# Optimization experiments

Hardware: AMD Instinct MI355X
Metric: run time of the kernel (lower is better)

Reference implementation:

```python
import jax, jax.numpy as jnp
import numpy as np
from jax import lax

B, HS, WS, C, NH, WIN = 32, 56, 56, 192, 6, 7
HID = int(C * 4.0)
EPS = 1e-5


def _ln(x, g, b):
    m = jnp.mean(x, -1, keepdims=True)
    v = jnp.mean((x - m) ** 2, -1, keepdims=True)
    return (x - m) * jax.lax.rsqrt(v + EPS) * g + b


def _cpe(x, H, W, w, b):
    # x: [B, H*W, C]; depthwise 3x3 conv positional encoding, residual add
    Bn = x.shape[0]
    feat = x.reshape(Bn, H, W, C).transpose(0, 3, 1, 2)  # NCHW
    out = lax.conv_general_dilated(feat, w, (1, 1), 'SAME',
                                   feature_group_count=C,
                                   dimension_numbers=('NCHW', 'OIHW', 'NCHW'))
    out = out + b[None, :, None, None]
    pos = out.transpose(0, 2, 3, 1).reshape(Bn, H * W, C)
    return x + pos


def _window_attn(xw, qkv_w, qkv_b, proj_w, proj_b):
    # xw: [nW, N, C]; faithful einops split 'b n (d k h) -> k b h n d'
    nW, N, _ = xw.shape
    hd = C // NH
    qkv = xw @ qkv_w + qkv_b                      # [nW, N, 3C]
    qkv = qkv.reshape(nW, N, hd, 3, NH)           # (d k h) split
    q, k, v = jnp.moveaxis(qkv.transpose(3, 0, 4, 1, 2), 0, 0)  # each [nW, NH, N, hd]
    scale = hd ** -0.5
    scores = jnp.einsum('bhid,bhjd->bhij', q, k) * scale
    attn = jax.nn.softmax(scores, axis=-1)
    out = jnp.einsum('bhij,bhjd->bhid', attn, v)  # [nW, NH, N, hd]
    out = out.transpose(0, 2, 1, 3).reshape(nW, N, C)  # 'b h n d -> b n (h d)'
    return out @ proj_w + proj_b


def _forward(x, H, W, cpe0_w, cpe0_b, cpe1_w, cpe1_b, n1_g, n1_b,
             qkv_w, qkv_b, proj_w, proj_b, n2_g, n2_b,
             fc1_w, fc1_b, fc2_w, fc2_b):
    Bn = x.shape[0]
    shortcut = _cpe(x, H, W, cpe0_w, cpe0_b)
    y = _ln(shortcut, n1_g, n1_b).reshape(Bn, H, W, C)
    pad_r = (WIN - W % WIN) % WIN
    pad_b = (WIN - H % WIN) % WIN
    y = jnp.pad(y, ((0, 0), (0, pad_b), (0, pad_r), (0, 0)))
    Hp, Wp = H + pad_b, W + pad_r
    nh, nw = Hp // WIN, Wp // WIN
    # faithful: 'b (w_h nw_h) (w_w nw_w) c -> (b nw_h nw_w) (w_h w_w) c'
    y = y.reshape(Bn, WIN, nh, WIN, nw, C).transpose(0, 2, 4, 1, 3, 5)
    y = y.reshape(Bn * nh * nw, WIN * WIN, C)
    y = _window_attn(y, qkv_w, qkv_b, proj_w, proj_b)
    # reverse: '(b nw_h nw_w) (w_h w_w) c -> b (w_h nw_h) (w_w nw_w) c'
    y = y.reshape(Bn, nh, nw, WIN, WIN, C).transpose(0, 3, 1, 4, 2, 5)
    y = y.reshape(Bn, Hp, Wp, C)[:, :H, :W, :].reshape(Bn, H * W, C)
    y = shortcut + y
    y = _cpe(y, H, W, cpe1_w, cpe1_b)
    h = _ln(y, n2_g, n2_b)
    h = jax.nn.gelu(h @ fc1_w + fc1_b, approximate=False) @ fc2_w + fc2_b
    return y + h


def setup_inputs() -> dict:
    key = jax.random.key(0)
    ks = jax.random.split(key, 12)
    s = 0.02
    return {
        'x': jax.random.normal(ks[0], (B, HS * WS, C), jnp.float32),
        'H': HS, 'W': WS,
        'cpe0_w': jax.random.normal(ks[1], (C, 1, 3, 3), jnp.float32) * s,
        'cpe0_b': jnp.zeros((C,), jnp.float32),
        'cpe1_w': jax.random.normal(ks[2], (C, 1, 3, 3), jnp.float32) * s,
        'cpe1_b': jnp.zeros((C,), jnp.float32),
        'n1_g': jnp.ones((C,), jnp.float32), 'n1_b': jnp.zeros((C,), jnp.float32),
        'qkv_w': jax.random.normal(ks[3], (C, 3 * C), jnp.float32) * s,
        'qkv_b': jnp.zeros((3 * C,), jnp.float32),
        'proj_w': jax.random.normal(ks[4], (C, C), jnp.float32) * s,
        'proj_b': jnp.zeros((C,), jnp.float32),
        'n2_g': jnp.ones((C,), jnp.float32), 'n2_b': jnp.zeros((C,), jnp.float32),
        'fc1_w': jax.random.normal(ks[5], (C, HID), jnp.float32) * s,
        'fc1_b': jnp.zeros((HID,), jnp.float32),
        'fc2_w': jax.random.normal(ks[6], (HID, C), jnp.float32) * s,
        'fc2_b': jnp.zeros((C,), jnp.float32),
    }


def reference(x, H, W, cpe0_w, cpe0_b, cpe1_w, cpe1_b, n1_g, n1_b,
              qkv_w, qkv_b, proj_w, proj_b, n2_g, n2_b,
              fc1_w, fc1_b, fc2_w, fc2_b):
    return _forward(x, H, W, cpe0_w, cpe0_b, cpe1_w, cpe1_b, n1_g, n1_b,
                    qkv_w, qkv_b, proj_w, proj_b, n2_g, n2_b,
                    fc1_w, fc1_b, fc2_w, fc2_b)
```

## Files before the change

### kernel.cpp

```cpp
#include <hip/hip_runtime.h>
#include <hip/hip_bf16.h>
#include <math.h>

#define Bn   32
#define Hh   56
#define Wd   56
#define Cc   192
#define NHh  6
#define HDim 32
#define HIDN 768
#define Tt   (Bn*Hh*Wd)
#define NWIN (Bn*64)

typedef __attribute__((ext_vector_type(8))) short short8;
typedef __attribute__((ext_vector_type(4))) short s4v;
typedef __attribute__((ext_vector_type(4))) float floatx4;

__device__ __forceinline__ short f2bf(float f) {
    unsigned u = __float_as_uint(f);
    u += 0x7fffu + ((u >> 16) & 1u);
    return (short)(u >> 16);
}
__device__ __forceinline__ float bf2f(short s) {
    return __uint_as_float(((unsigned)(unsigned short)s) << 16);
}

__device__ __forceinline__ void gl_lds16(const short* g, short* l) {
    __builtin_amdgcn_global_load_lds(
        (const __attribute__((address_space(1))) unsigned int*)g,
        (__attribute__((address_space(3))) unsigned int*)l,
        16, 0, 0);
}

__device__ __forceinline__ int xcd_swz(int bid, int nb) {
    return (bid & 7) * (nb >> 3) + (bid >> 3);
}

__global__ void k_transpose(const float* __restrict__ W, short* __restrict__ WT,
                            int K, int N) {
    int idx = blockIdx.x * 256 + threadIdx.x;
    if (idx >= K * N) return;
    int n = idx / K, k = idx % K;
    WT[idx] = f2bf(W[k * N + n]);
}

__global__ void k_transpose_qkv(const float* __restrict__ W, short* __restrict__ WT) {
    int idx = blockIdx.x * 256 + threadIdx.x;
    if (idx >= 192 * 576) return;
    int n = idx / 192, kk = idx % 192;
    int d = n & 31, hh = (n >> 5) % 6, k3 = n / 192;
    int oc = d * 18 + k3 * 6 + hh;
    WT[idx] = f2bf(W[kk * 576 + oc]);
}

template<int ADDP>
__global__ void __launch_bounds__(256) k_cpe_ln(
    const float* __restrict__ xin, const float* __restrict__ wconv,
    const float* __restrict__ bconv, const float* __restrict__ g,
    const float* __restrict__ beta, float* __restrict__ ysum_out,
    short* __restrict__ ln_out, int windowed, const short* __restrict__ proj)
{
    const int lane = threadIdx.x & 63;
    const int wv   = threadIdx.x >> 6;
    const bool act = lane < 48;
    const int c4   = (lane < 48 ? lane : lane - 16) * 4;

    const floatx4 zf = {0.f, 0.f, 0.f, 0.f};
    float wreg[36];
    #pragma unroll
    for (int i = 0; i < 9; ++i)
        *(floatx4*)&wreg[i * 4] = *(const floatx4*)(wconv + c4 * 9 + i * 4);
    const floatx4 gv  = *(const floatx4*)(g + c4);
    const floatx4 bv  = *(const floatx4*)(beta + c4);
    const floatx4 bcv = *(const floatx4*)(bconv + c4);

    const int W = xcd_swz(blockIdx.x, gridDim.x) * 4 + wv;
    const int b = W / (Hh * 7);
    const int rem = W % (Hh * 7);
    const int h = rem / 7, wslot = rem % 7;
    const int w0 = wslot * 8;

    floatx4 r[3][10];
    const int hy0 = (h > 0) ? h - 1 : 0;
    const int hy2 = (h < Hh - 1) ? h + 1 : Hh - 1;
    const int hys[3] = {hy0, h, hy2};
    #pragma unroll
    for (int dy = 0; dy < 3; ++dy) {
        const int hy = hys[dy];
        const float* rp = xin + ((size_t)b * (Hh * Wd) + hy * Wd) * Cc + c4;
        #pragma unroll
        for (int j = 0; j < 10; ++j) {
            int wx = w0 - 1 + j;
            int wc = (wx < 0) ? 0 : ((wx > Wd - 1) ? Wd - 1 : wx);
            floatx4 v = *(const floatx4*)(rp + wc * Cc);
            if (ADDP) {
                int prow = (b * 64 + (hy & 7) * 8 + (wc & 7)) * 49
                         + (hy >> 3) * 7 + (wc >> 3);
                s4v pv = *(const s4v*)(proj + (size_t)prow * Cc + c4);
                #pragma unroll
                for (int q = 0; q < 4; ++q) v[q] += bf2f(pv[q]);
            }
            r[dy][j] = v;
        }
    }
    if (h == 0) {
        #pragma unroll
        for (int j = 0; j < 10; ++j) r[0][j] = zf;
    }
    if (h == Hh - 1) {
        #pragma unroll
        for (int j = 0; j < 10; ++j) r[2][j] = zf;
    }
    if (w0 == 0)      { r[0][0] = zf; r[1][0] = zf; r[2][0] = zf; }
    if (w0 == Wd - 8) { r[0][9] = zf; r[1][9] = zf; r[2][9] = zf; }

    floatx4 val[8];
    #pragma unroll
    for (int tk = 0; tk < 8; ++tk) {
        floatx4 a = bcv;
        #pragma unroll
        for (int dy = 0; dy < 3; ++dy) {
            #pragma unroll
            for (int dx = 0; dx < 3; ++dx) {
                const int t = dy * 3 + dx;
                floatx4 v = r[dy][tk + dx];
                #pragma unroll
                for (int j = 0; j < 4; ++j)
                    a[j] += wreg[j * 9 + t] * v[j];
            }
        }
        floatx4 xc = r[1][tk + 1];
        #pragma unroll
        for (int j = 0; j < 4; ++j) val[tk][j] = xc[j] + a[j];
    }

    float s[8], s2[8];
    #pragma unroll
    for (int tk = 0; tk < 8; ++tk) {
        float a = val[tk][0] + val[tk][1] + val[tk][2] + val[tk][3];
        float a2 = val[tk][0]*val[tk][0] + val[tk][1]*val[tk][1]
                 + val[tk][2]*val[tk][2] + val[tk][3]*val[tk][3];
        s[tk]  = act ? a  : 0.f;
        s2[tk] = act ? a2 : 0.f;
    }
    #pragma unroll
    for (int off = 1; off < 64; off <<= 1) {
        #pragma unroll
        for (int tk = 0; tk < 8; ++tk) {
            s[tk]  += __shfl_xor(s[tk],  off, 64);
            s2[tk] += __shfl_xor(s2[tk], off, 64);
        }
    }

    const int blk0 = (b * Hh + h) * Wd + w0;
    #pragma unroll
    for (int tk = 0; tk < 8; ++tk) {
        const float mean = s[tk] * (1.0f / Cc);
        const float var  = s2[tk] * (1.0f / Cc) - mean * mean;
        const float rs   = rsqrtf(var + 1e-5f);
        int rr;
        if (windowed) {
            int win = b * 64 + (h & 7) * 8 + tk;
            int pos = (h >> 3) * 7 + wslot;
            rr = win * 49 + pos;
        } else {
            rr = blk0 + tk;
        }
        if (act) {
            *(floatx4*)(ysum_out + (size_t)(blk0 + tk) * Cc + c4) = val[tk];
            s4v o;
            #pragma unroll
            for (int j = 0; j < 4; ++j)
                o[j] = f2bf((val[tk][j] - mean) * rs * gv[j] + bv[j]);
            *(s4v*)(ln_out + (size_t)rr * Cc + c4) = o;
        }
    }
}

template<int K, int EPI>
__global__ void __launch_bounds__(256) k_gemm_tiled(
    const short* __restrict__ A, const short* __restrict__ BT,
    const float* __restrict__ bias, void* __restrict__ outp)
{
    __shared__ __align__(16) short As[128 * 32];
    __shared__ __align__(16) short Bs[64 * 32];
    const int tid = threadIdx.x;
    const int gx = gridDim.x;
    const int flat = blockIdx.y * gx + blockIdx.x;
    const int swz = xcd_swz(flat, gx * gridDim.y);
    const int n0 = (swz % gx) * 64;
    const int m0 = (swz / gx) * 128;
    const int w = tid >> 6, lane = tid & 63;
    const int lcol = lane & 15, quad = lane >> 4;

    floatx4 acc[2][4];
    #pragma unroll
    for (int mi = 0; mi < 2; ++mi)
        #pragma unroll
        for (int ni = 0; ni < 4; ++ni) acc[mi][ni] = (floatx4){0, 0, 0, 0};

    const int ar = tid >> 2;
    const int ac = (((tid & 3) ^ ((tid >> 2) & 3) ^ ((tid >> 4) & 3)) * 8);
    const short* agp  = A + (size_t)(m0 + ar) * K + ac;
    const short* agp2 = A + (size_t)(m0 + 64 + ar) * K + ac;
    const short* bgp  = BT + (size_t)(n0 + ar) * K + ac;
    short* asw = As + tid * 8;
    short* bsw = Bs + tid * 8;

    const int rsz = (quad ^ (lcol & 3) ^ ((lcol >> 2) & 3)) * 8;
    const short* ard0 = As + (w * 32 + lcol) * 32 + rsz;
    const short* ard1 = As + (w * 32 + 16 + lcol) * 32 + rsz;
    const short* brd  = Bs + lcol * 32 + rsz;

    for (int k0 = 0; k0 < K; k0 += 32) {
        __syncthreads();
        gl_lds16(agp + k0, asw);
        gl_lds16(agp2 + k0, asw + 64 * 32);
        gl_lds16(bgp + k0, bsw);
        __syncthreads();
        short8 a0 = *(const short8*)ard0;
        short8 a1 = *(const short8*)ard1;
        #pragma unroll
        for (int ni = 0; ni < 4; ++ni) {
            short8 b = *(const short8*)(brd + ni * 16 * 32);
            acc[0][ni] = __builtin_amdgcn_mfma_f32_16x16x32_bf16(a0, b, acc[0][ni], 0, 0, 0);
            acc[1][ni] = __builtin_amdgcn_mfma_f32_16x16x32_bf16(a1, b, acc[1][ni], 0, 0, 0);
        }
    }

    #pragma unroll
    for (int mi = 0; mi < 2; ++mi) {
        #pragma unroll
        for (int ni = 0; ni < 4; ++ni) {
            int col = n0 + ni * 16 + lcol;
            float bv;
            if (EPI == 0) {
                int d = col & 31, hh = (col >> 5) % 6, k3 = col / 192;
                bv = bias[d * 18 + k3 * 6 + hh];
            } else {
                bv = bias[col];
            }
            #pragma unroll
            for (int t = 0; t < 4; ++t) {
                int row = m0 + w * 32 + mi * 16 + quad * 4 + t;
                float v = acc[mi][ni][t] + bv;
                if (EPI == 0) {
                    ((short*)outp)[(size_t)row * 576 + col] = f2bf(v);
                } else if (EPI == 2) {
                    float gl = 0.5f * v * (1.0f + erff(v * 0.70710678118654752f));
                    ((short*)outp)[(size_t)row * HIDN + col] = f2bf(gl);
                } else if (EPI == 3) {
                    ((float*)outp)[(size_t)row * Cc + col] += v;
                } else {
                    ((short*)outp)[(size_t)row * Cc + col] = f2bf(v);
                }
            }
        }
    }
}

__global__ void __launch_bounds__(64) k_attn(
    const short* __restrict__ C, short* __restrict__ aout)
{
    int h = blockIdx.x, win = blockIdx.y;
    int lane = threadIdx.x;
    int lcol = lane & 15, quad = lane >> 4;
    __shared__ __align__(16) short buf[7424];
    short* Q  = buf;
    short* Kb = buf + 2560;
    short* Vt = buf + 5120;
    short* P  = buf;

    const short8 z8 = {0, 0, 0, 0, 0, 0, 0, 0};
    const size_t wbase = (size_t)win * 49 * 576;
    const int hq = h * 32;
    const int pr = lane >> 2, d8 = (lane & 3) * 8;

    #pragma unroll
    for (int it = 0; it < 4; ++it) {
        int pp = pr + it * 16;
        bool ok = pp < 49;
        size_t ro = wbase + (size_t)(ok ? pp : 0) * 576 + hq + d8;
        short8 vq = ok ? *(const short8*)(C + ro)       : z8;
        short8 vk = ok ? *(const short8*)(C + ro + 192) : z8;
        *(short8*)(Q  + pp * 40 + d8) = vq;
        *(short8*)(Kb + pp * 40 + d8) = vk;
    }
    #pragma unroll
    for (int it = 0; it < 4; ++it) {
        int pp = pr + it * 16;
        bool ok = pp < 49;
        size_t ro = wbase + (size_t)(ok ? pp : 0) * 576 + 384 + hq + d8;
        short8 vv = ok ? *(const short8*)(C + ro) : z8;
        #pragma unroll
        for (int j = 0; j < 8; ++j)
            Vt[(d8 + j) * 72 + pp] = vv[j];
    }

    floatx4 s[4][4];
    #pragma unroll
    for (int mi = 0; mi < 4; ++mi) {
        short8 aq = *(const short8*)(Q + (mi * 16 + lcol) * 40 + quad * 8);
        #pragma unroll
        for (int ni = 0; ni < 4; ++ni) {
            short8 bk = *(const short8*)(Kb + (ni * 16 + lcol) * 40 + quad * 8);
            floatx4 z = {0, 0, 0, 0};
            s[mi][ni] = __builtin_amdgcn_mfma_f32_16x16x32_bf16(aq, bk, z, 0, 0, 0);
        }
    }

    const float scale = 0.17677669529663688f;
    #pragma unroll
    for (int mi = 0; mi < 4; ++mi) {
        #pragma unroll
        for (int reg = 0; reg < 4; ++reg) {
            float vv[4];
            float mx = -3e38f;
            #pragma unroll
            for (int ni = 0; ni < 4; ++ni) {
                int col = ni * 16 + lcol;
                float v = (col < 49) ? s[mi][ni][reg] * scale : -3e38f;
                vv[ni] = v;
                mx = fmaxf(mx, v);
            }
            #pragma unroll
            for (int off = 1; off < 16; off <<= 1)
                mx = fmaxf(mx, __shfl_xor(mx, off, 64));
            float sum = 0.f;
            #pragma unroll
            for (int ni = 0; ni < 4; ++ni) {
                int col = ni * 16 + lcol;
                float e = (col < 49) ? __expf(vv[ni] - mx) : 0.f;
                vv[ni] = e;
                sum += e;
            }
            #pragma unroll
            for (int off = 1; off < 16; off <<= 1)
                sum += __shfl_xor(sum, off, 64);
            float inv = 1.0f / sum;
            int row = mi * 16 + quad * 4 + reg;
            #pragma unroll
            for (int ni = 0; ni < 4; ++ni)
                P[row * 72 + ni * 16 + lcol] = f2bf(vv[ni] * inv);
        }
    }

    #pragma unroll
    for (int mi = 0; mi < 4; ++mi) {
        short8 a0 = *(const short8*)(P + (mi * 16 + lcol) * 72 + quad * 8);
        short8 a1 = *(const short8*)(P + (mi * 16 + lcol) * 72 + 32 + quad * 8);
        #pragma unroll
        for (int nd = 0; nd < 2; ++nd) {
            short8 b0 = *(const short8*)(Vt + (nd * 16 + lcol) * 72 + quad * 8);
            short8 b1 = *(const short8*)(Vt + (nd * 16 + lcol) * 72 + 32 + quad * 8);
            floatx4 z = {0, 0, 0, 0};
            floatx4 o = __builtin_amdgcn_mfma_f32_16x16x32_bf16(a0, b0, z, 0, 0, 0);
            o = __builtin_amdgcn_mfma_f32_16x16x32_bf16(a1, b1, o, 0, 0, 0);
            #pragma unroll
            for (int reg = 0; reg < 4; ++reg) {
                int row = mi * 16 + quad * 4 + reg;
                if (row < 49)
                    aout[((size_t)win * 49 + row) * Cc + h * HDim + nd * 16 + lcol] =
                        f2bf(o[reg]);
            }
        }
    }
}

extern "C" void kernel_launch(void* const* d_in, const int* in_sizes, int n_in,
                              void* d_out, int out_size, void* d_ws, size_t ws_size,
                              hipStream_t stream)
{
    (void)in_sizes; (void)n_in; (void)out_size; (void)ws_size;
    const float* x      = (const float*)d_in[0];
    const float* cpe0_w = (const float*)d_in[3];
    const float* cpe0_b = (const float*)d_in[4];
    const float* cpe1_w = (const float*)d_in[5];
    const float* cpe1_b = (const float*)d_in[6];
    const float* n1_g   = (const float*)d_in[7];
    const float* n1_b   = (const float*)d_in[8];
    const float* qkv_w  = (const float*)d_in[9];
    const float* qkv_b  = (const float*)d_in[10];
    const float* proj_w = (const float*)d_in[11];
    const float* proj_b = (const float*)d_in[12];
    const float* n2_g   = (const float*)d_in[13];
    const float* n2_b   = (const float*)d_in[14];
    const float* fc1_w  = (const float*)d_in[15];
    const float* fc1_b  = (const float*)d_in[16];
    const float* fc2_w  = (const float*)d_in[17];
    const float* fc2_b  = (const float*)d_in[18];
    float* out = (float*)d_out;

    char* ws = (char*)d_ws;
    float* shortcut = (float*)ws;
    short* lnbuf    = (short*)(ws + 77070336);
    short* qkvbuf   = (short*)(ws + 115605504);
    short* attnout  = (short*)(ws + 231211008);
    short* projbuf  = qkvbuf;
    short* h1       = qkvbuf;
    short* wqkvT    = (short*)(ws + 269746176);
    short* wprojT   = (short*)(ws + 269967360);
    short* wfc1T    = (short*)(ws + 270041088);
    short* wfc2T    = (short*)(ws + 270336000);

    k_transpose_qkv<<<dim3((192 * 576 + 255) / 256), dim3(256), 0, stream>>>(qkv_w, wqkvT);
    k_transpose<<<dim3((192 * 192 + 255) / 256), dim3(256), 0, stream>>>(proj_w, wprojT, 192, 192);
    k_transpose<<<dim3((192 * 768 + 255) / 256), dim3(256), 0, stream>>>(fc1_w, wfc1T, 192, 768);
    k_transpose<<<dim3((768 * 192 + 255) / 256), dim3(256), 0, stream>>>(fc2_w, wfc2T, 768, 192);

    k_cpe_ln<0><<<dim3(Tt / 32), dim3(256), 0, stream>>>(x, cpe0_w, cpe0_b, n1_g, n1_b,
                                                         shortcut, lnbuf, 1, nullptr);
    k_gemm_tiled<192, 0><<<dim3(9, Tt / 128), dim3(256), 0, stream>>>(lnbuf, wqkvT, qkv_b, qkvbuf);
    k_attn<<<dim3(NHh, NWIN), dim3(64), 0, stream>>>(qkvbuf, attnout);
    k_gemm_tiled<192, 4><<<dim3(3, Tt / 128), dim3(256), 0, stream>>>(attnout, wprojT, proj_b, projbuf);
    k_cpe_ln<1><<<dim3(Tt / 32), dim3(256), 0, stream>>>(shortcut, cpe1_w, cpe1_b, n2_g, n2_b,
                                                         out, lnbuf, 0, projbuf);
    k_gemm_tiled<192, 2><<<dim3(12, Tt / 128), dim3(256), 0, stream>>>(lnbuf, wfc1T, fc1_b, h1);
    k_gemm_tiled<768, 3><<<dim3(3, Tt / 128), dim3(256), 0, stream>>>(h1, wfc2T, fc2_b, out);
}
```

Baseline: 557.2 us.

## Double-buffer LDS tiles in tiled GEMM and drop XOR swizzle

Turns the tiled bf16 MFMA GEMM's shared-memory staging into a two-stage ping-pong. The next K-slice is issued global-to-LDS while the current slice is consumed, leaving one barrier per iteration instead of two. It also removes the XOR swizzle on LDS write and read addresses and uses plain row-major offsets. This aims to hide global load latency behind MFMA work, but it doubles LDS use per block and may bring back LDS bank conflicts on the 64-byte-stride reads.

Measured after the change: 560.4 us. About the same (+0.6%).

```diff
diff --git a/kernel.cpp b/kernel.cpp
--- a/kernel.cpp
+++ b/kernel.cpp
@@ -182,8 +182,8 @@
     const short* __restrict__ A, const short* __restrict__ BT,
     const float* __restrict__ bias, void* __restrict__ outp)
 {
-    __shared__ __align__(16) short As[128 * 32];
-    __shared__ __align__(16) short Bs[64 * 32];
+    __shared__ __align__(16) short As[2][128 * 32];
+    __shared__ __align__(16) short Bs[2][64 * 32];
     const int tid = threadIdx.x;
     const int gx = gridDim.x;
     const int flat = blockIdx.y * gx + blockIdx.x;
@@ -199,32 +199,34 @@
         #pragma unroll
         for (int ni = 0; ni < 4; ++ni) acc[mi][ni] = (floatx4){0, 0, 0, 0};
 
-    const int ar = tid >> 2;
-    const int ac = (((tid & 3) ^ ((tid >> 2) & 3) ^ ((tid >> 4) & 3)) * 8);
+    const int ar = tid >> 2, ac = (tid & 3) * 8;
     const short* agp  = A + (size_t)(m0 + ar) * K + ac;
     const short* agp2 = A + (size_t)(m0 + 64 + ar) * K + ac;
     const short* bgp  = BT + (size_t)(n0 + ar) * K + ac;
-    short* asw = As + tid * 8;
-    short* bsw = Bs + tid * 8;
-
-    const int rsz = (quad ^ (lcol & 3) ^ ((lcol >> 2) & 3)) * 8;
-    const short* ard0 = As + (w * 32 + lcol) * 32 + rsz;
-    const short* ard1 = As + (w * 32 + 16 + lcol) * 32 + rsz;
-    const short* brd  = Bs + lcol * 32 + rsz;
-
-    for (int k0 = 0; k0 < K; k0 += 32) {
+
+    const int aoff = w * 32 + lcol;
+
+    gl_lds16(agp, &As[0][tid * 8]);
+    gl_lds16(agp2, &As[0][64 * 32 + tid * 8]);
+    gl_lds16(bgp, &Bs[0][tid * 8]);
+
+    #pragma unroll 2
+    for (int t = 0; t < K / 32; ++t) {
+        const int b = t & 1;
         __syncthreads();
-        gl_lds16(agp + k0, asw);
-        gl_lds16(agp2 + k0, asw + 64 * 32);
-        gl_lds16(bgp + k0, bsw);
-        __syncthreads();
-        short8 a0 = *(const short8*)ard0;
-        short8 a1 = *(const short8*)ard1;
+        if (t + 1 < K / 32) {
+            const int k1 = (t + 1) * 32;
+            gl_lds16(agp + k1, &As[b ^ 1][tid * 8]);
+            gl_lds16(agp2 + k1, &As[b ^ 1][64 * 32 + tid * 8]);
+            gl_lds16(bgp + k1, &Bs[b ^ 1][tid * 8]);
+        }
+        short8 a0 = *(const short8*)&As[b][aoff * 32 + quad * 8];
+        short8 a1 = *(const short8*)&As[b][(aoff + 16) * 32 + quad * 8];
         #pragma unroll
         for (int ni = 0; ni < 4; ++ni) {
-            short8 b = *(const short8*)(brd + ni * 16 * 32);
-            acc[0][ni] = __builtin_amdgcn_mfma_f32_16x16x32_bf16(a0, b, acc[0][ni], 0, 0, 0);
-            acc[1][ni] = __builtin_amdgcn_mfma_f32_16x16x32_bf16(a1, b, acc[1][ni], 0, 0, 0);
+            short8 bb = *(const short8*)&Bs[b][(ni * 16 + lcol) * 32 + quad * 8];
+            acc[0][ni] = __builtin_amdgcn_mfma_f32_16x16x32_bf16(a0, bb, acc[0][ni], 0, 0, 0);
+            acc[1][ni] = __builtin_amdgcn_mfma_f32_16x16x32_bf16(a1, bb, acc[1][ni], 0, 0, 0);
         }
     }
 
```
